# Optimization experiments

Hardware: AMD Instinct MI355X
Metric: run time of the kernel (lower is better)

Reference implementation:

```python
import jax, jax.numpy as jnp
import numpy as np

SL, BS, E, H, PF, STRIDE, SHIFT = 2048, 2, 1024, 16, 16, 1, 0
DH = E // H  # 64


def setup_inputs() -> dict:
    key = jax.random.key(0)
    ks = jax.random.split(key, 6)
    s = 0.02
    return {
        'x': jax.random.normal(ks[0], (SL, BS, E), jnp.float32),
        'ln_g': jnp.ones((E,), jnp.float32),
        'ln_b': jnp.zeros((E,), jnp.float32),
        'Wq': jax.random.normal(ks[1], (E, E), jnp.float32) * s,
        'bq': jnp.zeros((E,), jnp.float32),
        'Wk': jax.random.normal(ks[2], (E, E), jnp.float32) * s,
        'bk': jnp.zeros((E,), jnp.float32),
        'Wv': jax.random.normal(ks[3], (E, E), jnp.float32) * s,
        'bv': jnp.zeros((E,), jnp.float32),
        'Wo': jax.random.normal(ks[4], (E, E), jnp.float32) * s,
        'bo': jnp.zeros((E,), jnp.float32),
    }


def _layernorm(x, g, b, eps=1e-5):
    m = x.mean(-1, keepdims=True)
    v = jnp.var(x, axis=-1, keepdims=True)
    return (x - m) * jax.lax.rsqrt(v + eps) * g + b


def _sparsify(context, h):
    # faithful to sparsify(): r = (arange(h)+1)*stride - pf + shift (+ arange(pf)), mod c
    c = context.shape[0]
    base = (jnp.arange(h) + 1) * STRIDE - PF + SHIFT          # [h]
    idx = (base[None, :] + jnp.arange(PF)[:, None]) % c       # [pf, h]
    return context[idx.reshape(-1)].reshape(PF, h, context.shape[1], context.shape[2])


def reference(x, ln_g, ln_b, Wq, bq, Wk, bk, Wv, bv, Wo, bo):
    sl, bs, e = x.shape
    residual = x
    xn = _layernorm(x, ln_g, ln_b)
    # gather pf-sized local context window per query position (modular wrap)
    fetch = _sparsify(xn, sl)                                  # [pf, sl, bs, E]
    # per-token query (length-1) attending to its pf gathered keys
    q = (xn @ Wq + bq).reshape(sl, bs, H, DH)                  # [sl,bs,H,dh]
    k = (fetch @ Wk + bk).reshape(PF, sl, bs, H, DH)           # [pf,sl,bs,H,dh]
    v = (fetch @ Wv + bv).reshape(PF, sl, bs, H, DH)
    scale = 1.0 / jnp.sqrt(jnp.float32(DH))
    scores = jnp.einsum('sbhd,psbhd->sbhp', q, k) * scale      # [sl,bs,H,pf]
    attn = jax.nn.softmax(scores, axis=-1)
    out = jnp.einsum('sbhp,psbhd->sbhd', attn, v).reshape(sl, bs, e)
    out = out @ Wo + bo                                        # output projection
    # dropout is a no-op in eval
    return residual + out
```

## Files before the change

### kernel.cpp

```cpp
#include <hip/hip_runtime.h>
#include <cstdint>
#include <cstddef>

#define SLEN 2048
#define BSZ  2
#define EDIM 1024
#define NHEAD 16
#define DHEAD 64
#define PFW  16
#define NTOK (SLEN*BSZ)

typedef __attribute__((ext_vector_type(8))) short short8;
typedef __attribute__((ext_vector_type(4))) float floatx4;
typedef __attribute__((ext_vector_type(4))) int   int4v;

__device__ __forceinline__ short f2bf(float f) {
  union { float f; uint32_t u; } v; v.f = f;
  uint32_t r = v.u + 0x7fffu + ((v.u >> 16) & 1u);
  return (short)(r >> 16);
}
__device__ __forceinline__ float bf2f(short s) {
  union { uint32_t u; float f; } v; v.u = ((uint32_t)(uint16_t)s) << 16;
  return v.f;
}
__device__ __forceinline__ int q8(float f, float inv) {
  int q = __float2int_rn(f * inv);
  return min(127, max(-127, q));
}

__device__ __forceinline__ void async16(const void* g, void* l) {
  __builtin_amdgcn_global_load_lds((const __attribute__((address_space(1))) void*)g,
                                   (__attribute__((address_space(3))) void*)l,
                                   16, 0, 0);
}

#define VMCNT(n) asm volatile("s_waitcnt vmcnt(" #n ")" ::: "memory")

__global__ __launch_bounds__(256) void prep_kernel(
    const float* __restrict__ x, const float* __restrict__ g,
    const float* __restrict__ b, char* __restrict__ xn_i8,
    float* __restrict__ xn_scl,
    const float* __restrict__ W0, const float* __restrict__ W1,
    const float* __restrict__ W2, const float* __restrict__ W3,
    short* __restrict__ Wt_base)
{
  const int bid = blockIdx.x;
  const int tid = threadIdx.x;

  if (bid < NTOK) {
    const int row = bid;
    const float4 v = ((const float4*)(x + (size_t)row * EDIM))[tid];
    float s  = v.x + v.y + v.z + v.w;
    float ss = v.x * v.x + v.y * v.y + v.z * v.z + v.w * v.w;
#pragma unroll
    for (int off = 32; off; off >>= 1) {
      s  += __shfl_xor(s, off);
      ss += __shfl_xor(ss, off);
    }
    __shared__ float ws_s[4], ws_ss[4], ws_m[4];
    const int lane = tid & 63, wave = tid >> 6;
    if (lane == 0) { ws_s[wave] = s; ws_ss[wave] = ss; }
    __syncthreads();
    s  = ws_s[0] + ws_s[1] + ws_s[2] + ws_s[3];
    ss = ws_ss[0] + ws_ss[1] + ws_ss[2] + ws_ss[3];

    const float mean = s * (1.0f / EDIM);
    const float var  = ss * (1.0f / EDIM) - mean * mean;
    const float rs   = rsqrtf(var + 1e-5f);

    const float4 gv = ((const float4*)g)[tid];
    const float4 bv = ((const float4*)b)[tid];
    const float n0 = (v.x - mean) * rs * gv.x + bv.x;
    const float n1 = (v.y - mean) * rs * gv.y + bv.y;
    const float n2 = (v.z - mean) * rs * gv.z + bv.z;
    const float n3 = (v.w - mean) * rs * gv.w + bv.w;

    float am = fmaxf(fmaxf(fabsf(n0), fabsf(n1)), fmaxf(fabsf(n2), fabsf(n3)));
#pragma unroll
    for (int off = 32; off; off >>= 1) am = fmaxf(am, __shfl_xor(am, off));
    if (lane == 0) ws_m[wave] = am;
    __syncthreads();
    am = fmaxf(fmaxf(ws_m[0], ws_m[1]), fmaxf(ws_m[2], ws_m[3]));

    const float inv = (am > 1e-30f) ? 127.0f / am : 0.0f;
    const int q0 = q8(n0, inv), q1 = q8(n1, inv), q2 = q8(n2, inv), q3 = q8(n3, inv);
    const uint32_t pack = (uint32_t)(q0 & 0xff) | ((uint32_t)(q1 & 0xff) << 8) |
                          ((uint32_t)(q2 & 0xff) << 16) | ((uint32_t)(q3 & 0xff) << 24);
    ((uint32_t*)(xn_i8 + (size_t)row * EDIM))[tid] = pack;
    if (tid == 0) xn_scl[row] = am * (1.0f / 127.0f);
  } else {
    const int t = bid - NTOK;
    const int z = t >> 10;
    const int rem = t & 1023;
    const int n0 = (rem & 31) * 32;
    const int k0 = (rem >> 5) * 32;
    const float* W = (z == 0) ? W0 : (z == 1) ? W1 : (z == 2) ? W2 : W3;
    short* Wt = Wt_base + (size_t)z * EDIM * EDIM;

    __shared__ float tile[32][33];
    const int tx = tid & 31;
    const int ty = tid >> 5;
#pragma unroll
    for (int i = 0; i < 4; ++i)
      tile[ty + i * 8][tx] = W[(size_t)(k0 + ty + i * 8) * EDIM + n0 + tx];
    __syncthreads();
#pragma unroll
    for (int i = 0; i < 4; ++i)
      Wt[(size_t)(n0 + ty + i * 8) * EDIM + k0 + tx] = f2bf(tile[tx][ty + i * 8]);
  }
}

__global__ __launch_bounds__(256) void quant_w(
    const short* __restrict__ Wt, char* __restrict__ w_i8,
    float* __restrict__ w_scl)
{
  const int R = blockIdx.x;
  const int tid = threadIdx.x;
  const short4 s4 = ((const short4*)(Wt + (size_t)R * EDIM))[tid];
  const float w0 = bf2f(s4.x), w1 = bf2f(s4.y), w2 = bf2f(s4.z), w3 = bf2f(s4.w);

  float am = fmaxf(fmaxf(fabsf(w0), fabsf(w1)), fmaxf(fabsf(w2), fabsf(w3)));
#pragma unroll
  for (int off = 32; off; off >>= 1) am = fmaxf(am, __shfl_xor(am, off));
  __shared__ float wm[4];
  const int lane = tid & 63, wave = tid >> 6;
  if (lane == 0) wm[wave] = am;
  __syncthreads();
  am = fmaxf(fmaxf(wm[0], wm[1]), fmaxf(wm[2], wm[3]));

  const float inv = (am > 1e-30f) ? 127.0f / am : 0.0f;
  const int q0 = q8(w0, inv), q1 = q8(w1, inv), q2 = q8(w2, inv), q3 = q8(w3, inv);
  const uint32_t pack = (uint32_t)(q0 & 0xff) | ((uint32_t)(q1 & 0xff) << 8) |
                        ((uint32_t)(q2 & 0xff) << 16) | ((uint32_t)(q3 & 0xff) << 24);
  ((uint32_t*)(w_i8 + (size_t)R * EDIM))[tid] = pack;
  if (tid == 0) w_scl[R] = am * (1.0f / 127.0f);
}

__global__ __launch_bounds__(512, 2) void gemm_qkv256(
    const char* __restrict__ xn_i8, const float* __restrict__ xn_scl,
    const char* __restrict__ w_i8, const float* __restrict__ w_scl,
    const float* __restrict__ bq, const float* __restrict__ bk,
    const float* __restrict__ bv, short* __restrict__ qkv_base)
{
  __shared__ __align__(16) char lds[4][32768];

  const int bid = blockIdx.x;
  const int lin = (bid & 7) * 24 + (bid >> 3);
  const int mt  = lin & 15;
  const int nt  = lin >> 4;
  const int z   = nt >> 2;
  const int bm  = mt * 256;
  const int bnz = (nt & 3) * 256;

  const float* bias = (z == 0) ? bq : (z == 1) ? bk : bv;
  short* out = qkv_base + (size_t)z * NTOK * EDIM;

  const int tid = threadIdx.x;
  const int wv  = tid >> 6;
  const int ln  = tid & 63;
  const int q   = ln >> 4;
  const int l16 = ln & 15;
  const int wm  = wv >> 2;
  const int wn  = wv & 3;

  const int sr = tid >> 2;
  const int sc = ((tid & 3) * 16) ^ ((sr & 3) * 16);
  const char* gA0 = xn_i8 + (size_t)(bm + sr) * EDIM + sc;
  const char* gA1 = gA0 + (size_t)128 * EDIM;
  const char* gB0 = w_i8 + ((size_t)z << 20) + (size_t)(bnz + sr) * EDIM + sc;
  const char* gB1 = gB0 + (size_t)128 * EDIM;
  const int wbase = wv * 1024;

#define QSTAGE(tt) do { \
    char* s_ = lds[(tt) & 3]; \
    async16(gA0 + (tt) * 64, s_ + wbase); \
    async16(gA1 + (tt) * 64, s_ + 8192 + wbase); \
    async16(gB0 + (tt) * 64, s_ + 16384 + wbase); \
    async16(gB1 + (tt) * 64, s_ + 24576 + wbase); \
  } while (0)

  const int swz  = (q * 16) ^ ((l16 & 3) * 16);
  const int aoff = (wm * 128 + l16) * 64 + swz;
  const int boff = 16384 + (wn * 64 + l16) * 64 + swz;

  int4v acc[8][4];
#pragma unroll
  for (int mi = 0; mi < 8; ++mi)
#pragma unroll
    for (int ni = 0; ni < 4; ++ni) { int4v zz = {0, 0, 0, 0}; acc[mi][ni] = zz; }

  QSTAGE(0); QSTAGE(1); QSTAGE(2);
  VMCNT(8);
  __builtin_amdgcn_s_barrier();
  __builtin_amdgcn_sched_barrier(0);

#pragma unroll
  for (int t = 0; t < 16; ++t) {
    if (t + 3 < 16) QSTAGE(t + 3);

    const char* sl = lds[t & 3];
    int4v bf[4], af[8];
#pragma unroll
    for (int ni = 0; ni < 4; ++ni)
      bf[ni] = *(const int4v*)(sl + boff + ni * 1024);
#pragma unroll
    for (int mi = 0; mi < 8; ++mi)
      af[mi] = *(const int4v*)(sl + aoff + mi * 1024);

    __builtin_amdgcn_s_setprio(1);
#pragma unroll
    for (int mi = 0; mi < 8; ++mi)
#pragma unroll
      for (int ni = 0; ni < 4; ++ni)
        acc[mi][ni] = __builtin_amdgcn_mfma_i32_16x16x64_i8(
            af[mi], bf[ni], acc[mi][ni], 0, 0, 0);
    __builtin_amdgcn_s_setprio(0);

    if (t < 15) {
      if (t <= 12)      VMCNT(8);
      else if (t == 13) VMCNT(4);
      else              VMCNT(0);
      __builtin_amdgcn_s_barrier();
      __builtin_amdgcn_sched_barrier(0);
    }
  }
#undef QSTAGE

  const int rbase = bm + wm * 128 + q * 4;
  const int cbl   = bnz + wn * 64 + l16;
#pragma unroll
  for (int mi = 0; mi < 8; ++mi) {
    float sa[4];
#pragma unroll
    for (int r = 0; r < 4; ++r) sa[r] = xn_scl[rbase + mi * 16 + r];
#pragma unroll
    for (int ni = 0; ni < 4; ++ni) {
      const int c  = cbl + ni * 16;
      const float sb = w_scl[z * EDIM + c];
      const float bb = bias[c];
      const int4v v = acc[mi][ni];
#pragma unroll
      for (int r = 0; r < 4; ++r)
        out[(size_t)(rbase + mi * 16 + r) * EDIM + c] =
            f2bf((float)v[r] * (sa[r] * sb) + bb);
    }
  }
}

__global__ __launch_bounds__(256) void gemm_o_bf16(
    const short* __restrict__ Abf, const short* __restrict__ Bt,
    const float* __restrict__ bo, const float* __restrict__ residual,
    float* __restrict__ out)
{
  __shared__ __align__(16) char ring[4][12288];

  const int bm = blockIdx.x * 64;
  const int bn = blockIdx.y * 128;
  const int tid  = threadIdx.x;
  const int lane = tid & 63;
  const int wave = tid >> 6;

  const int lrow = lane >> 2;
  const int scol = ((lane & 3) * 16) ^ ((lrow & 3) * 16);
  const char* gA0 = (const char*)Abf + (size_t)(bm + wave * 16 + lrow) * (EDIM * 2) + scol;
  const char* gB0 = (const char*)Bt  + (size_t)(bn + wave * 32 + lrow) * (EDIM * 2) + scol;
  const char* gB1 = gB0 + (size_t)16 * (EDIM * 2);
  const int aw = wave * 1024;
  const int bw = 4096 + wave * 2048;

#define OSTAGE(tt) do { \
    char* s_ = ring[(tt) & 3]; \
    async16(gA0 + (tt) * 64, s_ + aw); \
    async16(gB0 + (tt) * 64, s_ + bw); \
    async16(gB1 + (tt) * 64, s_ + bw + 1024); \
  } while (0)

  const int wm  = (wave >> 1) * 32;
  const int wn  = (wave & 1) * 64;
  const int l16 = lane & 15;
  const int q4  = lane >> 4;
  const int swz  = (q4 * 16) ^ ((l16 & 3) * 16);
  const int aoff = (wm + l16) * 64 + swz;
  const int boff = 4096 + (wn + l16) * 64 + swz;

  floatx4 facc[2][4];
#pragma unroll
  for (int i = 0; i < 2; ++i)
#pragma unroll
    for (int j = 0; j < 4; ++j) { floatx4 zz = {0.f, 0.f, 0.f, 0.f}; facc[i][j] = zz; }

  OSTAGE(0); OSTAGE(1); OSTAGE(2);
  VMCNT(6);
  __builtin_amdgcn_s_barrier();
  __builtin_amdgcn_sched_barrier(0);

#pragma unroll
  for (int t = 0; t < 32; ++t) {
    if (t + 3 < 32) OSTAGE(t + 3);

    const char* sl = ring[t & 3];
    short8 af[2], bf[4];
#pragma unroll
    for (int mi = 0; mi < 2; ++mi)
      af[mi] = *(const short8*)(sl + aoff + mi * 1024);
#pragma unroll
    for (int ni = 0; ni < 4; ++ni)
      bf[ni] = *(const short8*)(sl + boff + ni * 1024);

    __builtin_amdgcn_s_setprio(1);
#pragma unroll
    for (int mi = 0; mi < 2; ++mi)
#pragma unroll
      for (int ni = 0; ni < 4; ++ni)
        facc[mi][ni] = __builtin_amdgcn_mfma_f32_16x16x32_bf16(
            af[mi], bf[ni], facc[mi][ni], 0, 0, 0);
    __builtin_amdgcn_s_setprio(0);

    if (t < 31) {
      if (t <= 28)      VMCNT(6);
      else if (t == 29) VMCNT(3);
      else              VMCNT(0);
      __builtin_amdgcn_s_barrier();
      __builtin_amdgcn_sched_barrier(0);
    }
  }
#undef OSTAGE

  const int r0 = bm + wm + q4 * 4;
  const int c0 = bn + wn + l16;
#pragma unroll
  for (int mi = 0; mi < 2; ++mi)
#pragma unroll
    for (int ni = 0; ni < 4; ++ni) {
      const int col = c0 + ni * 16;
      const float bb = bo[col];
#pragma unroll
      for (int r = 0; r < 4; ++r) {
        const int row = r0 + mi * 16 + r;
        const size_t idx = (size_t)row * EDIM + col;
        out[idx] = residual[idx] + facc[mi][ni][r] + bb;
      }
    }
}

#define VT_LD 80
#define PB_LD 40

__global__ __launch_bounds__(256) void attn_mfma(
    const short* __restrict__ Q, const short* __restrict__ K,
    const short* __restrict__ V, short* __restrict__ Obf)
{
  const int tid  = threadIdx.x;
  const int lane = tid & 63;
  const int wave = tid >> 6;
  const int quad = lane >> 4;
  const int l16  = lane & 15;

  const int bh = blockIdx.y;
  const int h  = bh & (NHEAD - 1);
  const int b  = bh >> 4;
  const int s_blk = blockIdx.x * 64;
  const int col0  = h * DHEAD;

  __shared__ __align__(16) short VT[64 * VT_LD];
  __shared__ __align__(16) short Pb[4][16 * PB_LD];

  for (int task = tid; task < 320; task += 256) {
    const int kp  = task >> 3;
    const int dg  = task & 7;
    const int kk0 = kp * 2;
    int sA = s_blk - 15 + kk0;
    int sB = sA + 1;
    if (sA < 0) sA += SLEN;  if (sA >= SLEN) sA -= SLEN;
    if (sB < 0) sB += SLEN;  if (sB >= SLEN) sB -= SLEN;
    const short8 vA = *(const short8*)(V + (size_t)(sA * BSZ + b) * EDIM + col0 + dg * 8);
    const short8 vB = *(const short8*)(V + (size_t)(sB * BSZ + b) * EDIM + col0 + dg * 8);
#pragma unroll
    for (int j = 0; j < 8; ++j) {
      const int d = dg * 8 + j;
      const uint32_t pack = (uint32_t)(uint16_t)vA[j] | ((uint32_t)(uint16_t)vB[j] << 16);
      *(uint32_t*)&VT[d * VT_LD + kk0] = pack;
    }
  }

  const int sw = s_blk + wave * 16;
  short8 aq[2];
  {
    const size_t base = (size_t)((sw + l16) * BSZ + b) * EDIM + col0 + quad * 8;
    aq[0] = *(const short8*)(Q + base);
    aq[1] = *(const short8*)(Q + base + 32);
  }
  short8 bkf[2][2];
#pragma unroll
  for (int T = 0; T < 2; ++T) {
    int ks = sw - 15 + T * 16 + l16;
    if (ks < 0) ks += SLEN;
    if (ks >= SLEN) ks -= SLEN;
    const size_t base = (size_t)(ks * BSZ + b) * EDIM + col0 + quad * 8;
    bkf[T][0] = *(const short8*)(K + base);
    bkf[T][1] = *(const short8*)(K + base + 32);
  }

  floatx4 S[2];
  { floatx4 zz = {0.f, 0.f, 0.f, 0.f}; S[0] = zz; S[1] = zz; }
#pragma unroll
  for (int T = 0; T < 2; ++T) {
    S[T] = __builtin_amdgcn_mfma_f32_16x16x32_bf16(aq[0], bkf[T][0], S[T], 0, 0, 0);
    S[T] = __builtin_amdgcn_mfma_f32_16x16x32_bf16(aq[1], bkf[T][1], S[T], 0, 0, 0);
  }

  float sc[2][4];
#pragma unroll
  for (int T = 0; T < 2; ++T)
#pragma unroll
    for (int r = 0; r < 4; ++r) {
      const int m = quad * 4 + r;
      const int c = T * 16 + l16;
      const int d = c - m;
      sc[T][r] = (d >= 0 && d <= 15) ? S[T][r] * 0.125f : -1e30f;
    }
  float mx[4], sm[4];
#pragma unroll
  for (int r = 0; r < 4; ++r) mx[r] = fmaxf(sc[0][r], sc[1][r]);
#pragma unroll
  for (int off = 1; off <= 8; off <<= 1)
#pragma unroll
    for (int r = 0; r < 4; ++r) mx[r] = fmaxf(mx[r], __shfl_xor(mx[r], off));
  float p[2][4];
#pragma unroll
  for (int r = 0; r < 4; ++r) {
    p[0][r] = __expf(sc[0][r] - mx[r]);
    p[1][r] = __expf(sc[1][r] - mx[r]);
    sm[r] = p[0][r] + p[1][r];
  }
#pragma unroll
  for (int off = 1; off <= 8; off <<= 1)
#pragma unroll
    for (int r = 0; r < 4; ++r) sm[r] += __shfl_xor(sm[r], off);

  __syncthreads();

  short* Pw = Pb[wave];
#pragma unroll
  for (int T = 0; T < 2; ++T)
#pragma unroll
    for (int r = 0; r < 4; ++r) {
      const int m = quad * 4 + r;
      const int c = T * 16 + l16;
      Pw[m * PB_LD + c] = f2bf(p[T][r]);
    }
  __syncthreads();
  const short8 ap = *(const short8*)(Pw + l16 * PB_LD + quad * 8);

  floatx4 Oacc[4];
  { floatx4 zz = {0.f, 0.f, 0.f, 0.f}; Oacc[0] = zz; Oacc[1] = zz; Oacc[2] = zz; Oacc[3] = zz; }
#pragma unroll
  for (int nt = 0; nt < 4; ++nt) {
    const short8 bv = *(const short8*)(VT + (nt * 16 + l16) * VT_LD + wave * 16 + quad * 8);
    Oacc[nt] = __builtin_amdgcn_mfma_f32_16x16x32_bf16(ap, bv, Oacc[nt], 0, 0, 0);
  }

  float ism[4];
#pragma unroll
  for (int r = 0; r < 4; ++r) ism[r] = 1.0f / sm[r];
#pragma unroll
  for (int nt = 0; nt < 4; ++nt)
#pragma unroll
    for (int r = 0; r < 4; ++r) {
      const int m = quad * 4 + r;
      const int row = (sw + m) * BSZ + b;
      Obf[(size_t)row * EDIM + col0 + nt * 16 + l16] = f2bf(Oacc[nt][r] * ism[r]);
    }
}

extern "C" void kernel_launch(void* const* d_in, const int* in_sizes, int n_in,
                              void* d_out, int out_size, void* d_ws, size_t ws_size,
                              hipStream_t stream) {
  const float* x    = (const float*)d_in[0];
  const float* ln_g = (const float*)d_in[1];
  const float* ln_b = (const float*)d_in[2];
  const float* Wq   = (const float*)d_in[3];
  const float* bq   = (const float*)d_in[4];
  const float* Wk   = (const float*)d_in[5];
  const float* bk   = (const float*)d_in[6];
  const float* Wv   = (const float*)d_in[7];
  const float* bv   = (const float*)d_in[8];
  const float* Wo   = (const float*)d_in[9];
  const float* bo   = (const float*)d_in[10];
  float* out = (float*)d_out;

  char* ws = (char*)d_ws;
  char*  xn_i8   = ws;
  short* Wt      = (short*)(ws + ((size_t)4  << 20));
  char*  w_i8    = ws + ((size_t)12 << 20);
  short* QKV     = (short*)(ws + ((size_t)16 << 20));
  float* xn_scl  = (float*)(ws + ((size_t)44 << 20));
  float* w_scl   = (float*)(ws + ((size_t)44 << 20) + (1 << 16));
  short* Obf     = (short*)ws;

  prep_kernel<<<NTOK + 4096, 256, 0, stream>>>(x, ln_g, ln_b, xn_i8, xn_scl,
                                               Wq, Wk, Wv, Wo, Wt);
  quant_w<<<3 * EDIM, 256, 0, stream>>>(Wt, w_i8, w_scl);
  gemm_qkv256<<<192, 512, 0, stream>>>(xn_i8, xn_scl, w_i8, w_scl,
                                       bq, bk, bv, QKV);
  attn_mfma<<<dim3(SLEN / 64, BSZ * NHEAD), 256, 0, stream>>>(
      QKV, QKV + (size_t)NTOK * EDIM, QKV + (size_t)2 * NTOK * EDIM, Obf);
  gemm_o_bf16<<<dim3(NTOK / 64, EDIM / 128), 256, 0, stream>>>(
      Obf, Wt + (size_t)3 * EDIM * EDIM, bo, x, out);
}
```

Before: 149.2 us.

## Retile output projection GEMM to 128x128 tiles with 512 threads

Replaces the 64x128 output-projection GEMM with a 128x128 tile kernel using 8 waves, K-step of 64 per stage and a 4-deep async LDS ring. Block indices are remapped so neighbouring blocks share A/B panels in cache. Larger tiles raise arithmetic intensity per LDS/global load but halve the number of blocks and raise LDS use, which can reduce occupancy and latency hiding.

```diff
diff --git a/kernel.cpp b/kernel.cpp
--- a/kernel.cpp
+++ b/kernel.cpp
@@ -7,7 +7,6 @@
 #define EDIM 1024
 #define NHEAD 16
 #define DHEAD 64
-#define PFW  16
 #define NTOK (SLEN*BSZ)
 
 typedef __attribute__((ext_vector_type(8))) short short8;
@@ -27,13 +26,11 @@
   int q = __float2int_rn(f * inv);
   return min(127, max(-127, q));
 }
-
 __device__ __forceinline__ void async16(const void* g, void* l) {
   __builtin_amdgcn_global_load_lds((const __attribute__((address_space(1))) void*)g,
                                    (__attribute__((address_space(3))) void*)l,
                                    16, 0, 0);
 }
-
 #define VMCNT(n) asm volatile("s_waitcnt vmcnt(" #n ")" ::: "memory")
 
 __global__ __launch_bounds__(256) void prep_kernel(
@@ -187,7 +184,7 @@
 #pragma unroll
   for (int mi = 0; mi < 8; ++mi)
 #pragma unroll
-    for (int ni = 0; ni < 4; ++ni) { int4v zz = {0, 0, 0, 0}; acc[mi][ni] = zz; }
+    for (int ni = 0; ni < 4; ++ni) { int4v zz = {0,0,0,0}; acc[mi][ni] = zz; }
 
   QSTAGE(0); QSTAGE(1); QSTAGE(2);
   VMCNT(8);
@@ -247,78 +244,92 @@
   }
 }
 
-__global__ __launch_bounds__(256) void gemm_o_bf16(
+__global__ __launch_bounds__(512, 2) void gemm_o128(
     const short* __restrict__ Abf, const short* __restrict__ Bt,
     const float* __restrict__ bo, const float* __restrict__ residual,
     float* __restrict__ out)
 {
-  __shared__ __align__(16) char ring[4][12288];
-
-  const int bm = blockIdx.x * 64;
-  const int bn = blockIdx.y * 128;
-  const int tid  = threadIdx.x;
-  const int lane = tid & 63;
-  const int wave = tid >> 6;
-
-  const int lrow = lane >> 2;
-  const int scol = ((lane & 3) * 16) ^ ((lrow & 3) * 16);
-  const char* gA0 = (const char*)Abf + (size_t)(bm + wave * 16 + lrow) * (EDIM * 2) + scol;
-  const char* gB0 = (const char*)Bt  + (size_t)(bn + wave * 32 + lrow) * (EDIM * 2) + scol;
-  const char* gB1 = gB0 + (size_t)16 * (EDIM * 2);
-  const int aw = wave * 1024;
-  const int bw = 4096 + wave * 2048;
+  __shared__ __align__(16) char lds[4][32768];
+
+  const int bid = blockIdx.x;
+  const int lin = (bid & 7) * 32 + (bid >> 3);
+  const int mt  = lin >> 3;
+  const int nt  = lin & 7;
+  const int bm  = mt * 128;
+  const int bn  = nt * 128;
+
+  const int tid = threadIdx.x;
+  const int wv  = tid >> 6;
+  const int ln  = tid & 63;
+  const int quad = ln >> 4;
+  const int l16  = ln & 15;
+  const int wm  = wv >> 2;
+  const int wn  = wv & 3;
+
+  const int sr = tid >> 3;
+  const int sc = ((tid & 7) * 16) ^ ((sr & 7) * 16);
+  const char* gA0 = (const char*)Abf + (size_t)(bm + sr) * 2048 + sc;
+  const char* gA1 = gA0 + (size_t)64 * 2048;
+  const char* gB0 = (const char*)Bt  + (size_t)(bn + sr) * 2048 + sc;
+  const char* gB1 = gB0 + (size_t)64 * 2048;
+  const int wbase = wv * 1024;
 
 #define OSTAGE(tt) do { \
-    char* s_ = ring[(tt) & 3]; \
-    async16(gA0 + (tt) * 64, s_ + aw); \
-    async16(gB0 + (tt) * 64, s_ + bw); \
-    async16(gB1 + (tt) * 64, s_ + bw + 1024); \
+    char* s_ = lds[(tt) & 3]; \
+    async16(gA0 + (tt) * 128, s_ + wbase); \
+    async16(gA1 + (tt) * 128, s_ + 8192 + wbase); \
+    async16(gB0 + (tt) * 128, s_ + 16384 + wbase); \
+    async16(gB1 + (tt) * 128, s_ + 24576 + wbase); \
   } while (0)
 
-  const int wm  = (wave >> 1) * 32;
-  const int wn  = (wave & 1) * 64;
-  const int l16 = lane & 15;
-  const int q4  = lane >> 4;
-  const int swz  = (q4 * 16) ^ ((l16 & 3) * 16);
-  const int aoff = (wm + l16) * 64 + swz;
-  const int boff = 4096 + (wn + l16) * 64 + swz;
-
-  floatx4 facc[2][4];
-#pragma unroll
-  for (int i = 0; i < 2; ++i)
-#pragma unroll
-    for (int j = 0; j < 4; ++j) { floatx4 zz = {0.f, 0.f, 0.f, 0.f}; facc[i][j] = zz; }
+  int aoff[2], boff[2];
+#pragma unroll
+  for (int ks = 0; ks < 2; ++ks) {
+    const int c = ks * 64 + quad * 16;
+    const int s = (l16 & 7) * 16;
+    aoff[ks] = (wm * 64 + l16) * 128 + (c ^ s);
+    boff[ks] = 16384 + (wn * 32 + l16) * 128 + (c ^ s);
+  }
+
+  floatx4 facc[4][2];
+#pragma unroll
+  for (int mi = 0; mi < 4; ++mi)
+#pragma unroll
+    for (int ni = 0; ni < 2; ++ni) { floatx4 zz = {0.f,0.f,0.f,0.f}; facc[mi][ni] = zz; }
 
   OSTAGE(0); OSTAGE(1); OSTAGE(2);
-  VMCNT(6);
+  VMCNT(8);
   __builtin_amdgcn_s_barrier();
   __builtin_amdgcn_sched_barrier(0);
 
 #pragma unroll
-  for (int t = 0; t < 32; ++t) {
-    if (t + 3 < 32) OSTAGE(t + 3);
-
-    const char* sl = ring[t & 3];
-    short8 af[2], bf[4];
-#pragma unroll
-    for (int mi = 0; mi < 2; ++mi)
-      af[mi] = *(const short8*)(sl + aoff + mi * 1024);
-#pragma unroll
-    for (int ni = 0; ni < 4; ++ni)
-      bf[ni] = *(const short8*)(sl + boff + ni * 1024);
-
-    __builtin_amdgcn_s_setprio(1);
-#pragma unroll
-    for (int mi = 0; mi < 2; ++mi)
-#pragma unroll
-      for (int ni = 0; ni < 4; ++ni)
-        facc[mi][ni] = __builtin_amdgcn_mfma_f32_16x16x32_bf16(
-            af[mi], bf[ni], facc[mi][ni], 0, 0, 0);
-    __builtin_amdgcn_s_setprio(0);
-
-    if (t < 31) {
-      if (t <= 28)      VMCNT(6);
-      else if (t == 29) VMCNT(3);
+  for (int t = 0; t < 16; ++t) {
+    if (t + 3 < 16) OSTAGE(t + 3);
+
+    const char* sl = lds[t & 3];
+#pragma unroll
+    for (int ks = 0; ks < 2; ++ks) {
+      short8 af[4], bf[2];
+#pragma unroll
+      for (int mi = 0; mi < 4; ++mi)
+        af[mi] = *(const short8*)(sl + aoff[ks] + mi * 2048);
+#pragma unroll
+      for (int ni = 0; ni < 2; ++ni)
+        bf[ni] = *(const short8*)(sl + boff[ks] + ni * 2048);
+
+      __builtin_amdgcn_s_setprio(1);
+#pragma unroll
+      for (int mi = 0; mi < 4; ++mi)
+#pragma unroll
+        for (int ni = 0; ni < 2; ++ni)
+          facc[mi][ni] = __builtin_amdgcn_mfma_f32_16x16x32_bf16(
+              af[mi], bf[ni], facc[mi][ni], 0, 0, 0);
+      __builtin_amdgcn_s_setprio(0);
+    }
+
+    if (t < 15) {
+      if (t <= 12)      VMCNT(8);
+      else if (t == 13) VMCNT(4);
       else              VMCNT(0);
       __builtin_amdgcn_s_barrier();
       __builtin_amdgcn_sched_barrier(0);
@@ -326,12 +337,12 @@
   }
 #undef OSTAGE
 
-  const int r0 = bm + wm + q4 * 4;
-  const int c0 = bn + wn + l16;
-#pragma unroll
-  for (int mi = 0; mi < 2; ++mi)
-#pragma unroll
-    for (int ni = 0; ni < 4; ++ni) {
+  const int r0 = bm + wm * 64 + quad * 4;
+  const int c0 = bn + wn * 32 + l16;
+#pragma unroll
+  for (int mi = 0; mi < 4; ++mi)
+#pragma unroll
+    for (int ni = 0; ni < 2; ++ni) {
       const int col = c0 + ni * 16;
       const float bb = bo[col];
 #pragma unroll
@@ -505,6 +516,6 @@
                                        bq, bk, bv, QKV);
   attn_mfma<<<dim3(SLEN / 64, BSZ * NHEAD), 256, 0, stream>>>(
       QKV, QKV + (size_t)NTOK * EDIM, QKV + (size_t)2 * NTOK * EDIM, Obf);
-  gemm_o_bf16<<<dim3(NTOK / 64, EDIM / 128), 256, 0, stream>>>(
+  gemm_o128<<<256, 512, 0, stream>>>(
       Obf, Wt + (size_t)3 * EDIM * EDIM, bo, x, out);
 }
```

After: 148.3 us. No clear change (-0.6%).
